# Optimization experiments

Measured on AMD Instinct MI355X. Metric: run time of the kernel, lower is better.

## Reference

```python
import jax, jax.numpy as jnp
import numpy as np

B, M, K, F_IN, H = 64, 1024, 16, 4, 64  # B graphs of M nodes each, k=16 neighbors


def _knn_idx(h):
    # h: [B, M, H] -> indices of K nearest neighbors (excluding self): [B, M, K]
    sq = jnp.sum(h * h, axis=-1)                                   # [B, M]
    d = sq[:, :, None] + sq[:, None, :] - 2.0 * jnp.einsum('bmf,bnf->bmn', h, h)
    d = jnp.where(jnp.eye(M, dtype=bool)[None], jnp.float32(jnp.inf), d)
    _, idx = jax.lax.top_k(-d, K)                                  # smallest distances
    return idx


def _edge_conv(h, w1, b1, w2, b2):
    # Dynamic-graph EdgeConv with max aggregation (PyG default):
    # msg = MLP(concat[x_i, x_j - x_i]); out_i = max_j msg
    idx = _knn_idx(h)                                              # [B, M, K]
    x_j = jax.vmap(lambda hb, ib: hb[ib])(h, idx)                  # [B, M, K, H]
    x_i = jnp.broadcast_to(h[:, :, None, :], x_j.shape)
    msg = jnp.concatenate([x_i, x_j - x_i], axis=-1)               # [B, M, K, 2H]
    msg = jax.nn.relu(msg @ w1 + b1) @ w2 + b2                     # [B, M, K, H]
    return jnp.max(msg, axis=2)                                    # [B, M, H]


def setup_inputs() -> dict:
    key = jax.random.key(0)
    ks = jax.random.split(key, 20)

    def lin(k, fi, fo):
        return jax.random.normal(k, (fi, fo), jnp.float32) / np.sqrt(fi)

    inp = {
        'x': jax.random.normal(ks[0], (B * M, F_IN), jnp.float32),
        'batch': jnp.repeat(jnp.arange(B, dtype=jnp.int64), M),
        # encoder: Linear(4,32) ReLU Linear(32,64) ReLU
        'enc_w1': lin(ks[1], F_IN, 32), 'enc_b1': jnp.zeros((32,), jnp.float32),
        'enc_w2': lin(ks[2], 32, H),    'enc_b2': jnp.zeros((H,), jnp.float32),
        # EdgeConv MLPs: Linear(128,64) ReLU Linear(64,64)
        'ec1_w1': lin(ks[3], 2 * H, H), 'ec1_b1': jnp.zeros((H,), jnp.float32),
        'ec1_w2': lin(ks[4], H, H),     'ec1_b2': jnp.zeros((H,), jnp.float32),
        'ec2_w1': lin(ks[5], 2 * H, H), 'ec2_b1': jnp.zeros((H,), jnp.float32),
        'ec2_w2': lin(ks[6], H, H),     'ec2_b2': jnp.zeros((H,), jnp.float32),
        # output MLP: Linear(64,32) ReLU Linear(32,1)
        'out_w1': lin(ks[7], H, 32),    'out_b1': jnp.zeros((32,), jnp.float32),
        'out_w2': lin(ks[8], 32, 1),    'out_b2': jnp.zeros((1,), jnp.float32),
    }
    return inp


def reference(x, batch, enc_w1, enc_b1, enc_w2, enc_b2,
              ec1_w1, ec1_b1, ec1_w2, ec1_b2,
              ec2_w1, ec2_b1, ec2_w2, ec2_b2,
              out_w1, out_b1, out_w2, out_b2):
    # batch is repeat(arange(B), M): equal-size graphs -> reshape into [B, M, .]
    h = jax.nn.relu(jax.nn.relu(x @ enc_w1 + enc_b1) @ enc_w2 + enc_b2)  # [N, 64]
    h = h.reshape(B, M, H)
    h = _edge_conv(h, ec1_w1, ec1_b1, ec1_w2, ec1_b2)
    h = _edge_conv(h, ec2_w1, ec2_b1, ec2_w2, ec2_b2)
    g = jnp.mean(h, axis=1)                                        # global_mean_pool -> [B, 64]
    out = jax.nn.relu(g @ out_w1 + out_b1) @ out_w2 + out_b2       # [B, 1]
    return out.reshape(-1)                                         # [B]
```

## Files before the change

kernel.cpp:

```cpp
#include <hip/hip_runtime.h>
#include <math.h>

#define B_ 64
#define M_ 1024
#define H_ 64
#define N_ (B_*M_)

typedef _Float16 half8 __attribute__((ext_vector_type(8)));
typedef float  floatx4 __attribute__((ext_vector_type(4)));

#define MFMA16(a,b,c) __builtin_amdgcn_mfma_f32_16x16x32_f16(a,b,c,0,0,0)
#define MED3(a,b,c)   __builtin_amdgcn_fmed3f(a,b,c)

__global__ __launch_bounds__(256) void enc_kernel(
    const float* __restrict__ x,
    const float* __restrict__ w1,
    const float* __restrict__ b1,
    const float* __restrict__ w2,
    const float* __restrict__ b2,
    float* __restrict__ h,
    _Float16* __restrict__ hhi,
    _Float16* __restrict__ hlo,
    float* __restrict__ sq)
{
    __shared__ float sw1[4*32];
    __shared__ float sb1[32];
    __shared__ float sw2[32*64];
    __shared__ float sb2[64];
    int t = threadIdx.x;
    for (int i = t; i < 128; i += 256) sw1[i] = w1[i];
    if (t < 32) sb1[t] = b1[t];
    for (int i = t; i < 2048; i += 256) sw2[i] = w2[i];
    if (t < 64) sb2[t] = b2[t];
    __syncthreads();
    int n = blockIdx.x * 256 + t;
    float4 xv = *(const float4*)(x + (size_t)n*4);
    float hid[32];
    #pragma unroll
    for (int o = 0; o < 32; ++o) {
        float a = sb1[o] + xv.x*sw1[0*32+o] + xv.y*sw1[1*32+o]
                        + xv.z*sw1[2*32+o] + xv.w*sw1[3*32+o];
        hid[o] = fmaxf(a, 0.f);
    }
    float* hout = h + (size_t)n*64;
    float sqa = 0.f;
    #pragma unroll 4
    for (int oc = 0; oc < 16; ++oc) {
        float4 acc = make_float4(sb2[oc*4+0], sb2[oc*4+1], sb2[oc*4+2], sb2[oc*4+3]);
        #pragma unroll
        for (int f = 0; f < 32; ++f) {
            float4 w = *(const float4*)(sw2 + f*64 + oc*4);
            float hv = hid[f];
            acc.x += hv*w.x; acc.y += hv*w.y; acc.z += hv*w.z; acc.w += hv*w.w;
        }
        acc.x = fmaxf(acc.x,0.f); acc.y = fmaxf(acc.y,0.f);
        acc.z = fmaxf(acc.z,0.f); acc.w = fmaxf(acc.w,0.f);
        *(float4*)(hout + oc*4) = acc;
        sqa += acc.x*acc.x + acc.y*acc.y + acc.z*acc.z + acc.w*acc.w;
        union { _Float16 f[4]; uint2 u; } Hh, Hl;
        Hh.f[0]=(_Float16)acc.x; Hh.f[1]=(_Float16)acc.y;
        Hh.f[2]=(_Float16)acc.z; Hh.f[3]=(_Float16)acc.w;
        Hl.f[0]=(_Float16)(acc.x-(float)Hh.f[0]); Hl.f[1]=(_Float16)(acc.y-(float)Hh.f[1]);
        Hl.f[2]=(_Float16)(acc.z-(float)Hh.f[2]); Hl.f[3]=(_Float16)(acc.w-(float)Hh.f[3]);
        *(uint2*)(hhi + (size_t)n*64 + oc*4) = Hh.u;
        *(uint2*)(hlo + (size_t)n*64 + oc*4) = Hl.u;
    }
    sq[n] = sqa;
}

__global__ __launch_bounds__(256) void convert_kernel(
    const float* __restrict__ h,
    _Float16* __restrict__ hhi, _Float16* __restrict__ hlo,
    float* __restrict__ sq)
{
    int t = threadIdx.x, lane = t & 63, w = t >> 6;
    int base = blockIdx.x * 64 + w * 16;
    for (int it = 0; it < 16; ++it) {
        int i = base + it;
        float v = h[(size_t)i*64 + lane];
        _Float16 hi = (_Float16)v;
        _Float16 lo = (_Float16)(v - (float)hi);
        hhi[(size_t)i*64 + lane] = hi;
        hlo[(size_t)i*64 + lane] = lo;
        float s = v*v;
        #pragma unroll
        for (int off = 1; off < 64; off <<= 1) s += __shfl_xor(s, off, 64);
        if (lane == 0) sq[i] = s;
    }
}

__global__ __launch_bounds__(256) void gemmA_kernel(
    const float* __restrict__ h,
    const float* __restrict__ w1,
    float* __restrict__ A)
{
    __shared__ float sw[64*64];
    int t = threadIdx.x;
    for (int idx = t; idx < 4096; idx += 256) sw[idx] = w1[4096 + idx];
    __syncthreads();
    int n = blockIdx.x * 256 + t;
    float4 hv[16];
    const float* src = h + (size_t)n*64;
    #pragma unroll
    for (int c = 0; c < 16; ++c) hv[c] = *(const float4*)(src + c*4);
    float* dst = A + (size_t)n*64;
    #pragma unroll 2
    for (int oc = 0; oc < 16; ++oc) {
        float4 acc = make_float4(0.f,0.f,0.f,0.f);
        #pragma unroll
        for (int f = 0; f < 64; ++f) {
            float xv = ((const float*)hv)[f];
            float4 w = *(const float4*)(sw + f*64 + oc*4);
            acc.x += xv*w.x; acc.y += xv*w.y; acc.z += xv*w.z; acc.w += xv*w.w;
        }
        *(float4*)(dst + oc*4) = acc;
    }
}

__global__ __launch_bounds__(512, 4) void knn_kernel(
    const _Float16* __restrict__ hhi,
    const _Float16* __restrict__ hlo,
    const float* __restrict__ sqg,
    unsigned short* __restrict__ knn)
{
    __shared__ __align__(16) _Float16 bufH[2][32*64];
    __shared__ __align__(16) _Float16 bufL[2][32*64];
    __shared__ __align__(16) float sqS[1024];
    __shared__ float md[128*65];

    int t = threadIdx.x, lane = t & 63, w = t >> 6;
    int bi = blockIdx.x;
    int g   = (bi & 7) | ((bi >> 6) << 3);
    int qt8 = (bi >> 3) & 7;
    const _Float16* hhig = hhi + (size_t)g*M_*64;
    const _Float16* hlog = hlo + (size_t)g*M_*64;
    const float*    sqb  = sqg + (size_t)g*M_;

    if (t < 256) ((float4*)sqS)[t] = ((const float4*)sqb)[t];

    int m16 = lane & 15, gid = lane >> 4;
    int crow = gid*4, koct = gid*8;
    int sw = m16 & 7;

    int u  = t & 255;
    int rr = u >> 3;
    int gl = u & 7;
    int pp = gl ^ (rr & 7);
    const _Float16* srcb = (t < 256 ? hhig : hlog) + rr*64 + gl*8;
    _Float16* dst0 = (t < 256 ? bufH[0] : bufL[0]) + rr*64 + pp*8;
    _Float16* dst1 = (t < 256 ? bufH[1] : bufL[1]) + rr*64 + pp*8;

    int qbase = qt8*128 + w*16;
    half8 Qh0, Qh1, Ql0, Ql1;
    {
        const _Float16* ph = hhig + (size_t)(qbase + m16)*64;
        const _Float16* pl = hlog + (size_t)(qbase + m16)*64;
        Qh0 = *(const half8*)(ph + koct);
        Qh1 = *(const half8*)(ph + 32 + koct);
        Ql0 = *(const half8*)(pl + koct);
        Ql1 = *(const half8*)(pl + 32 + koct);
    }

    float bd[16];
    #pragma unroll
    for (int k = 0; k < 16; ++k) bd[k] = INFINITY;

    int ts_self = qt8*8 + w;

    float4 a, b;
    a = *(const float4*)(srcb);
    b = *(const float4*)(srcb + 2048);
    *(float4*)dst0 = a;
    a = *(const float4*)(srcb + 2*2048);
    __syncthreads();

    float c1 = 1.f + sqS[qbase + m16];

    int o0 = m16*64 + ((gid ^ sw) * 8);
    int o1 = o0 ^ 32;

    auto insert4 = [&](floatx4 acc, float4 sqv, unsigned cid, bool st) {
        #pragma unroll
        for (int r = 0; r < 4; ++r) {
            float s  = fmaf(-2.f, acc[r], (&sqv.x)[r]);
            float t2 = c1 + s;
            unsigned kb = (__float_as_uint(t2) & 0xFFFFFC00u) | (cid + r);
            float fk = __uint_as_float(kb);
            if (st && (crow + r) == m16) fk = INFINITY;
            float nb0 = fminf(bd[0], fk);
            #pragma unroll
            for (int k = 15; k >= 1; --k) bd[k] = MED3(fk, bd[k-1], bd[k]);
            bd[0] = nb0;
        }
    };

    auto compute = [&](int T, const _Float16* bh, const _Float16* bl) {
        #pragma unroll
        for (int s = 0; s < 2; ++s) {
            int ob = s*1024;
            half8 Ah0 = *(const half8*)(bh + ob + o0);
            half8 Ah1 = *(const half8*)(bh + ob + o1);
            half8 Al0 = *(const half8*)(bl + ob + o0);
            half8 Al1 = *(const half8*)(bl + ob + o1);
            float4 sqv = *(const float4*)(sqS + T*32 + s*16 + crow);
            unsigned cid = (unsigned)(T*32 + s*16 + crow);
            bool st = (T*2 + s) == ts_self;
            floatx4 acc = {0.f, 0.f, 0.f, 0.f};
            acc = MFMA16(Ah0, Qh0, acc);
            acc = MFMA16(Ah1, Qh1, acc);
            acc = MFMA16(Ah0, Ql0, acc);
            acc = MFMA16(Ah1, Ql1, acc);
            acc = MFMA16(Al0, Qh0, acc);
            acc = MFMA16(Al1, Qh1, acc);
            insert4(acc, sqv, cid, st);
        }
    };

    #pragma unroll 1
    for (int T = 0; T < 32; T += 2) {
        __builtin_amdgcn_s_barrier();
        *(float4*)dst1 = b;
        b = *(const float4*)(srcb + (size_t)((T+3)&31)*2048);
        asm volatile("s_waitcnt lgkmcnt(0)" ::: "memory");
        __builtin_amdgcn_s_barrier();
        __builtin_amdgcn_sched_barrier(0);
        compute(T, bufH[0], bufL[0]);
        __builtin_amdgcn_s_barrier();
        *(float4*)dst0 = a;
        a = *(const float4*)(srcb + (size_t)((T+4)&31)*2048);
        asm volatile("s_waitcnt lgkmcnt(0)" ::: "memory");
        __builtin_amdgcn_s_barrier();
        __builtin_amdgcn_sched_barrier(0);
        compute(T+1, bufH[1], bufL[1]);
    }

    __syncthreads();
    int qrow = w*16 + m16;
    #pragma unroll
    for (int k = 0; k < 16; ++k) md[qrow*65 + gid*16 + k] = bd[k];
    __syncthreads();
    if (w < 2) {
        int q = w*64 + lane;
        float b2[16];
        #pragma unroll
        for (int k = 0; k < 16; ++k) b2[k] = INFINITY;
        const float* mrow = md + (size_t)q*65;
        #pragma unroll
        for (int c8 = 0; c8 < 8; ++c8) {
            float sv[8];
            #pragma unroll
            for (int j = 0; j < 8; ++j) sv[j] = mrow[c8*8 + j];
            #pragma unroll
            for (int j = 0; j < 8; ++j) {
                float s = sv[j];
                float nb0 = fminf(b2[0], s);
                #pragma unroll
                for (int k = 15; k >= 1; --k) b2[k] = MED3(s, b2[k-1], b2[k]);
                b2[0] = nb0;
            }
        }
        union { unsigned short us[16]; uint4 v4[2]; } o;
        #pragma unroll
        for (int k = 0; k < 16; ++k)
            o.us[k] = (unsigned short)(__float_as_uint(b2[k]) & 1023u);
        size_t gq = (size_t)g*M_ + qt8*128 + q;
        uint4* dst = (uint4*)(knn + gq*16);
        dst[0] = o.v4[0];
        dst[1] = o.v4[1];
    }
}

__global__ __launch_bounds__(256) void edge_kernel(
    const float* __restrict__ h,
    const float* __restrict__ A,
    const unsigned short* __restrict__ knn,
    const float* __restrict__ w1,
    const float* __restrict__ b1,
    const float* __restrict__ w2,
    const float* __restrict__ b2,
    float* __restrict__ hout)
{
    __shared__ __align__(16) _Float16 wdf[16*64*8];
    __shared__ __align__(16) _Float16 w2f[16*64*8];
    float* CsB = (float*)w2f;
    int t = threadIdx.x;
    for (int u = t; u < 512; u += 256) {
        int ulane = u & 63, nt = u >> 7, ks = (u >> 6) & 1;
        int n = nt*16 + (ulane & 15);
        int kbase = ks*32 + ((ulane >> 4) * 8);
        int fh = (((nt*2+ks)*2+0)*64 + ulane)*8;
        int fl = (((nt*2+ks)*2+1)*64 + ulane)*8;
        #pragma unroll
        for (int j = 0; j < 8; ++j) {
            int k = kbase + j;
            float vd = w1[k*64+n] - w1[4096 + k*64+n];
            _Float16 dh = (_Float16)vd;
            wdf[fh+j] = dh;
            wdf[fl+j] = (_Float16)(vd - (float)dh);
            float v2 = w2[k*64+n];
            _Float16 h2 = (_Float16)v2;
            w2f[fh+j] = h2;
            w2f[fl+j] = (_Float16)(v2 - (float)h2);
        }
    }
    __syncthreads();
    int lane = t & 63, wid = t >> 6;
    int m16 = lane & 15, gid = lane >> 4;
    int koct = gid*8, crow = gid*4;
    int bi = blockIdx.x;
    int g  = (bi & 7) | ((bi >> 7) << 3);
    int qt = (bi >> 3) & 15;
    int i0 = g*M_ + qt*64 + wid*16;
    const float* Ab = A + (size_t)g*M_*H_;

    half8 W2r[4][2][2];
    #pragma unroll
    for (int nt = 0; nt < 4; ++nt)
        #pragma unroll
        for (int ks = 0; ks < 2; ++ks)
            #pragma unroll
            for (int p = 0; p < 2; ++p)
                W2r[nt][ks][p] = *(const half8*)&w2f[(((nt*2+ks)*2+p)*64+lane)*8];

    float b1v[4];
    #pragma unroll
    for (int nt = 0; nt < 4; ++nt) b1v[nt] = b1[nt*16+m16];
    float b2v = b2[gid*16+m16];
    __syncthreads();

    half8 Hh[2], Hl[2];
    #pragma unroll
    for (int ks = 0; ks < 2; ++ks) {
        const float* hp = h + (size_t)(i0+m16)*64 + ks*32 + koct;
        float4 v0 = *(const float4*)hp;
        float4 v1 = *(const float4*)(hp+4);
        float va[8] = {v0.x,v0.y,v0.z,v0.w,v1.x,v1.y,v1.z,v1.w};
        #pragma unroll
        for (int j = 0; j < 8; ++j) {
            _Float16 hi = (_Float16)va[j];
            Hh[ks][j] = hi;
            Hl[ks][j] = (_Float16)(va[j]-(float)hi);
        }
    }
    #pragma unroll
    for (int nt = 0; nt < 4; ++nt) {
        floatx4 acc = {b1v[nt], b1v[nt], b1v[nt], b1v[nt]};
        #pragma unroll
        for (int ks = 0; ks < 2; ++ks) {
            half8 wh = *(const half8*)&wdf[(((nt*2+ks)*2+0)*64+lane)*8];
            half8 wl = *(const half8*)&wdf[(((nt*2+ks)*2+1)*64+lane)*8];
            acc = MFMA16(Hh[ks], wh, acc);
            acc = MFMA16(Hh[ks], wl, acc);
            acc = MFMA16(Hl[ks], wh, acc);
        }
        #pragma unroll
        for (int r = 0; r < 4; ++r)
            CsB[((wid*16) + crow + r)*64 + nt*16 + m16] = acc[r];
    }
    __syncthreads();

    const unsigned short* knb = knn + (size_t)i0*16;
    #pragma unroll 2
    for (int nn = 0; nn < 16; ++nn) {
        int j = knb[nn*16 + m16];
        const float* Ap = Ab + (size_t)j*64;
        half8 Mh[2], Ml[2];
        #pragma unroll
        for (int ks = 0; ks < 2; ++ks) {
            float4 a0 = *(const float4*)(Ap + ks*32 + koct);
            float4 a1 = *(const float4*)(Ap + ks*32 + koct + 4);
            const float* cp = &CsB[(wid*16 + nn)*64 + ks*32 + koct];
            float4 c0 = *(const float4*)cp;
            float4 c1 = *(const float4*)(cp+4);
            float mv[8] = {
                fmaxf(a0.x+c0.x,0.f), fmaxf(a0.y+c0.y,0.f),
                fmaxf(a0.z+c0.z,0.f), fmaxf(a0.w+c0.w,0.f),
                fmaxf(a1.x+c1.x,0.f), fmaxf(a1.y+c1.y,0.f),
                fmaxf(a1.z+c1.z,0.f), fmaxf(a1.w+c1.w,0.f)};
            #pragma unroll
            for (int jj = 0; jj < 8; ++jj) {
                _Float16 hi = (_Float16)mv[jj];
                Mh[ks][jj] = hi;
                Ml[ks][jj] = (_Float16)(mv[jj]-(float)hi);
            }
        }
        floatx4 acc[4];
        #pragma unroll
        for (int nt = 0; nt < 4; ++nt) {
            acc[nt] = (floatx4){0.f,0.f,0.f,0.f};
            #pragma unroll
            for (int ks = 0; ks < 2; ++ks) {
                acc[nt] = MFMA16(Mh[ks], W2r[nt][ks][0], acc[nt]);
                acc[nt] = MFMA16(Mh[ks], W2r[nt][ks][1], acc[nt]);
                acc[nt] = MFMA16(Ml[ks], W2r[nt][ks][0], acc[nt]);
            }
        }
        float om[4];
        #pragma unroll
        for (int nt = 0; nt < 4; ++nt) {
            float mr = fmaxf(fmaxf(acc[nt][0], acc[nt][1]),
                             fmaxf(acc[nt][2], acc[nt][3]));
            mr = fmaxf(mr, __shfl_xor(mr, 16, 64));
            mr = fmaxf(mr, __shfl_xor(mr, 32, 64));
            om[nt] = mr;
        }
        float val = (gid == 0) ? om[0] : (gid == 1) ? om[1]
                  : (gid == 2) ? om[2] : om[3];
        hout[(size_t)(i0+nn)*64 + gid*16 + m16] = val + b2v;
    }
}

__global__ __launch_bounds__(256) void pool_kernel(
    const float* __restrict__ h,
    const float* __restrict__ w1,
    const float* __restrict__ b1,
    const float* __restrict__ w2,
    const float* __restrict__ b2,
    float* __restrict__ out)
{
    __shared__ float part[4][64];
    __shared__ float g[64];
    __shared__ float hid[32];
    int t = threadIdx.x;
    int o = t & 63, p = t >> 6;
    int b = blockIdx.x;
    const float* hb = h + (size_t)b*M_*H_;
    float s = 0.f;
    for (int m = p; m < M_; m += 4) s += hb[(size_t)m*64 + o];
    part[p][o] = s;
    __syncthreads();
    if (t < 64) g[t] = (part[0][t] + part[1][t] + part[2][t] + part[3][t]) * (1.f/M_);
    __syncthreads();
    if (t < 32) {
        float a = b1[t];
        for (int f = 0; f < 64; ++f) a += g[f] * w1[f*32 + t];
        hid[t] = fmaxf(a, 0.f);
    }
    __syncthreads();
    if (t == 0) {
        float a = b2[0];
        for (int f = 0; f < 32; ++f) a += hid[f] * w2[f];
        out[b] = a;
    }
}

extern "C" void kernel_launch(void* const* d_in, const int* in_sizes, int n_in,
                              void* d_out, int out_size, void* d_ws, size_t ws_size,
                              hipStream_t stream)
{
    (void)in_sizes; (void)n_in; (void)out_size; (void)ws_size;
    const float* x      = (const float*)d_in[0];
    const float* enc_w1 = (const float*)d_in[2];
    const float* enc_b1 = (const float*)d_in[3];
    const float* enc_w2 = (const float*)d_in[4];
    const float* enc_b2 = (const float*)d_in[5];
    const float* ec1_w1 = (const float*)d_in[6];
    const float* ec1_b1 = (const float*)d_in[7];
    const float* ec1_w2 = (const float*)d_in[8];
    const float* ec1_b2 = (const float*)d_in[9];
    const float* ec2_w1 = (const float*)d_in[10];
    const float* ec2_b1 = (const float*)d_in[11];
    const float* ec2_w2 = (const float*)d_in[12];
    const float* ec2_b2 = (const float*)d_in[13];
    const float* out_w1 = (const float*)d_in[14];
    const float* out_b1 = (const float*)d_in[15];
    const float* out_w2 = (const float*)d_in[16];
    const float* out_b2 = (const float*)d_in[17];

    char* ws = (char*)d_ws;
    float*          h   = (float*)(ws);
    char*           r2  = ws + (size_t)N_*64*4;
    _Float16*       hhi = (_Float16*)r2;
    _Float16*       hlo = (_Float16*)(r2 + (size_t)N_*64*2);
    float*          A   = (float*)r2;
    unsigned short* idx = (unsigned short*)(ws + (size_t)N_*64*4*2);
    float*          sq  = (float*)(ws + (size_t)N_*64*4*2 + (size_t)N_*16*2);

    enc_kernel<<<N_/256, 256, 0, stream>>>(x, enc_w1, enc_b1, enc_w2, enc_b2,
                                           h, hhi, hlo, sq);
    knn_kernel <<<B_*8, 512, 0, stream>>>(hhi, hlo, sq, idx);
    gemmA_kernel<<<N_/256, 256, 0, stream>>>(h, ec1_w1, A);
    edge_kernel<<<N_/64, 256, 0, stream>>>(h, A, idx, ec1_w1, ec1_b1, ec1_w2, ec1_b2, h);
    convert_kernel<<<N_/64, 256, 0, stream>>>(h, hhi, hlo, sq);
    knn_kernel <<<B_*8, 512, 0, stream>>>(hhi, hlo, sq, idx);
    gemmA_kernel<<<N_/256, 256, 0, stream>>>(h, ec2_w1, A);
    edge_kernel<<<N_/64, 256, 0, stream>>>(h, A, idx, ec2_w1, ec2_b1, ec2_w2, ec2_b2, h);
    pool_kernel<<<B_, 256, 0, stream>>>(h, out_w1, out_b1, out_w2, out_b2, (float*)d_out);
}
```

Before: 404.1 us.

## Double candidate tile to 64 rows and use one barrier per kNN stage

The kNN kernel now stages 64 candidate rows per LDS buffer instead of 32, so the loop runs 16 iterations with 4 MFMA sub-tiles each. Each iteration writes the next tile into the other buffer while computing on the current one, and ends with a single barrier instead of two per tile. This halves the number of barriers and loop iterations and overlaps the LDS stores with compute. In exchange it doubles LDS usage for the staging buffers, which may lower occupancy, and keeps more global-load registers live.

New measurement: 403.2 us. About the same (-0.2%).

```diff
diff --git a/kernel.cpp b/kernel.cpp
--- a/kernel.cpp
+++ b/kernel.cpp
@@ -123,8 +123,8 @@
     const float* __restrict__ sqg,
     unsigned short* __restrict__ knn)
 {
-    __shared__ __align__(16) _Float16 bufH[2][32*64];
-    __shared__ __align__(16) _Float16 bufL[2][32*64];
+    __shared__ __align__(16) _Float16 bufH[2][64*64];
+    __shared__ __align__(16) _Float16 bufL[2][64*64];
     __shared__ __align__(16) float sqS[1024];
     __shared__ float md[128*65];
 
@@ -147,8 +147,8 @@
     int gl = u & 7;
     int pp = gl ^ (rr & 7);
     const _Float16* srcb = (t < 256 ? hhig : hlog) + rr*64 + gl*8;
-    _Float16* dst0 = (t < 256 ? bufH[0] : bufL[0]) + rr*64 + pp*8;
-    _Float16* dst1 = (t < 256 ? bufH[1] : bufL[1]) + rr*64 + pp*8;
+    _Float16* dstA = (t < 256 ? bufH[0] : bufL[0]) + rr*64 + pp*8;
+    _Float16* dstB = (t < 256 ? bufH[1] : bufL[1]) + rr*64 + pp*8;
 
     int qbase = qt8*128 + w*16;
     half8 Qh0, Qh1, Ql0, Ql1;
@@ -167,11 +167,11 @@
 
     int ts_self = qt8*8 + w;
 
-    float4 a, b;
-    a = *(const float4*)(srcb);
-    b = *(const float4*)(srcb + 2048);
-    *(float4*)dst0 = a;
-    a = *(const float4*)(srcb + 2*2048);
+    float4 p0 = *(const float4*)(srcb);
+    float4 p1 = *(const float4*)(srcb + 2048);
+    *(float4*)dstA = p0;  *(float4*)(dstA + 2048) = p1;
+    p0 = *(const float4*)(srcb + 4096);
+    p1 = *(const float4*)(srcb + 4096 + 2048);
     __syncthreads();
 
     float c1 = 1.f + sqS[qbase + m16];
@@ -196,15 +196,15 @@
 
     auto compute = [&](int T, const _Float16* bh, const _Float16* bl) {
         #pragma unroll
-        for (int s = 0; s < 2; ++s) {
+        for (int s = 0; s < 4; ++s) {
             int ob = s*1024;
             half8 Ah0 = *(const half8*)(bh + ob + o0);
             half8 Ah1 = *(const half8*)(bh + ob + o1);
             half8 Al0 = *(const half8*)(bl + ob + o0);
             half8 Al1 = *(const half8*)(bl + ob + o1);
-            float4 sqv = *(const float4*)(sqS + T*32 + s*16 + crow);
-            unsigned cid = (unsigned)(T*32 + s*16 + crow);
-            bool st = (T*2 + s) == ts_self;
+            float4 sqv = *(const float4*)(sqS + T*64 + s*16 + crow);
+            unsigned cid = (unsigned)(T*64 + s*16 + crow);
+            bool st = (T*4 + s) == ts_self;
             floatx4 acc = {0.f, 0.f, 0.f, 0.f};
             acc = MFMA16(Ah0, Qh0, acc);
             acc = MFMA16(Ah1, Qh1, acc);
@@ -217,24 +217,20 @@
     };
 
     #pragma unroll 1
-    for (int T = 0; T < 32; T += 2) {
-        __builtin_amdgcn_s_barrier();
-        *(float4*)dst1 = b;
-        b = *(const float4*)(srcb + (size_t)((T+3)&31)*2048);
+    for (int T = 0; T < 16; ++T) {
+        __builtin_amdgcn_sched_barrier(0);
+        _Float16* dw = (T & 1) ? dstA : dstB;
+        *(float4*)dw = p0;  *(float4*)(dw + 2048) = p1;
+        { size_t o = (size_t)((T+2)&15)*4096;
+          p0 = *(const float4*)(srcb + o);
+          p1 = *(const float4*)(srcb + o + 2048); }
+        const _Float16* bh = (T & 1) ? bufH[1] : bufH[0];
+        const _Float16* bl = (T & 1) ? bufL[1] : bufL[0];
+        compute(T, bh, bl);
         asm volatile("s_waitcnt lgkmcnt(0)" ::: "memory");
         __builtin_amdgcn_s_barrier();
-        __builtin_amdgcn_sched_barrier(0);
-        compute(T, bufH[0], bufL[0]);
-        __builtin_amdgcn_s_barrier();
-        *(float4*)dst0 = a;
-        a = *(const float4*)(srcb + (size_t)((T+4)&31)*2048);
-        asm volatile("s_waitcnt lgkmcnt(0)" ::: "memory");
-        __builtin_amdgcn_s_barrier();
-        __builtin_amdgcn_sched_barrier(0);
-        compute(T+1, bufH[1], bufL[1]);
-    }
-
-    __syncthreads();
+    }
+
     int qrow = w*16 + m16;
     #pragma unroll
     for (int k = 0; k < 16; ++k) md[qrow*65 + gid*16 + k] = bd[k];
```

## Shrink kNN blocks to 256 threads and merge top-k lists with shuffles

Applied to the files above, without the earlier changes.

The kNN kernel now uses 256-thread blocks covering 64 queries each, twice as many blocks, with each thread loading both the hi and lo fp16 tiles. The candidate-tile pipeline becomes one barrier per tile: the next tile is prefetched into registers while the current one is computed. The shared-memory merge of the four per-lane top-16 lists is replaced by two rounds of xor-shuffle exchange plus a bitonic merge in registers. The aim is to cut shared memory and barrier cost and raise occupancy, in exchange for reloading each graph's candidate data in twice as many blocks.

After: 411.0 us. Within noise of the previous version (+1.7%).

```diff
diff --git a/kernel.cpp b/kernel.cpp
--- a/kernel.cpp
+++ b/kernel.cpp
@@ -117,7 +117,7 @@
     }
 }
 
-__global__ __launch_bounds__(512, 4) void knn_kernel(
+__global__ __launch_bounds__(256, 6) void knn_kernel(
     const _Float16* __restrict__ hhi,
     const _Float16* __restrict__ hlo,
     const float* __restrict__ sqg,
@@ -126,31 +126,30 @@
     __shared__ __align__(16) _Float16 bufH[2][32*64];
     __shared__ __align__(16) _Float16 bufL[2][32*64];
     __shared__ __align__(16) float sqS[1024];
-    __shared__ float md[128*65];
 
     int t = threadIdx.x, lane = t & 63, w = t >> 6;
     int bi = blockIdx.x;
-    int g   = (bi & 7) | ((bi >> 6) << 3);
-    int qt8 = (bi >> 3) & 7;
+    int g  = (bi & 7) | ((bi >> 7) << 3);
+    int qt = (bi >> 3) & 15;
     const _Float16* hhig = hhi + (size_t)g*M_*64;
     const _Float16* hlog = hlo + (size_t)g*M_*64;
     const float*    sqb  = sqg + (size_t)g*M_;
 
-    if (t < 256) ((float4*)sqS)[t] = ((const float4*)sqb)[t];
+    ((float4*)sqS)[t] = ((const float4*)sqb)[t];
 
     int m16 = lane & 15, gid = lane >> 4;
     int crow = gid*4, koct = gid*8;
     int sw = m16 & 7;
 
-    int u  = t & 255;
-    int rr = u >> 3;
-    int gl = u & 7;
+    int rr = t >> 3;
+    int gl = t & 7;
     int pp = gl ^ (rr & 7);
-    const _Float16* srcb = (t < 256 ? hhig : hlog) + rr*64 + gl*8;
-    _Float16* dst0 = (t < 256 ? bufH[0] : bufL[0]) + rr*64 + pp*8;
-    _Float16* dst1 = (t < 256 ? bufH[1] : bufL[1]) + rr*64 + pp*8;
-
-    int qbase = qt8*128 + w*16;
+    const _Float16* srcH = hhig + rr*64 + gl*8;
+    const _Float16* srcL = hlog + rr*64 + gl*8;
+    _Float16* dstH = bufH[0] + rr*64 + pp*8;
+    _Float16* dstL = bufL[0] + rr*64 + pp*8;
+
+    int qbase = qt*64 + w*16;
     half8 Qh0, Qh1, Ql0, Ql1;
     {
         const _Float16* ph = hhig + (size_t)(qbase + m16)*64;
@@ -165,13 +164,14 @@
     #pragma unroll
     for (int k = 0; k < 16; ++k) bd[k] = INFINITY;
 
-    int ts_self = qt8*8 + w;
-
-    float4 a, b;
-    a = *(const float4*)(srcb);
-    b = *(const float4*)(srcb + 2048);
-    *(float4*)dst0 = a;
-    a = *(const float4*)(srcb + 2*2048);
+    int ts_self = qt*4 + w;
+
+    {
+        float4 h0 = *(const float4*)srcH;
+        float4 l0 = *(const float4*)srcL;
+        *(float4*)dstH = h0;
+        *(float4*)dstL = l0;
+    }
     __syncthreads();
 
     float c1 = 1.f + sqS[qbase + m16];
@@ -217,53 +217,47 @@
     };
 
     #pragma unroll 1
-    for (int T = 0; T < 32; T += 2) {
-        __builtin_amdgcn_s_barrier();
-        *(float4*)dst1 = b;
-        b = *(const float4*)(srcb + (size_t)((T+3)&31)*2048);
+    for (int T = 0; T < 32; ++T) {
+        size_t o = (size_t)((T+1) & 31) * 2048;
+        float4 h1 = *(const float4*)(srcH + o);
+        float4 l1 = *(const float4*)(srcL + o);
+        const _Float16* bh = (T & 1) ? bufH[1] : bufH[0];
+        const _Float16* bl = (T & 1) ? bufL[1] : bufL[0];
+        compute(T, bh, bl);
+        int sel = ((T & 1) ^ 1) * 2048;
+        *(float4*)(dstH + sel) = h1;
+        *(float4*)(dstL + sel) = l1;
         asm volatile("s_waitcnt lgkmcnt(0)" ::: "memory");
         __builtin_amdgcn_s_barrier();
-        __builtin_amdgcn_sched_barrier(0);
-        compute(T, bufH[0], bufL[0]);
-        __builtin_amdgcn_s_barrier();
-        *(float4*)dst0 = a;
-        a = *(const float4*)(srcb + (size_t)((T+4)&31)*2048);
-        asm volatile("s_waitcnt lgkmcnt(0)" ::: "memory");
-        __builtin_amdgcn_s_barrier();
-        __builtin_amdgcn_sched_barrier(0);
-        compute(T+1, bufH[1], bufL[1]);
-    }
-
-    __syncthreads();
-    int qrow = w*16 + m16;
-    #pragma unroll
-    for (int k = 0; k < 16; ++k) md[qrow*65 + gid*16 + k] = bd[k];
-    __syncthreads();
-    if (w < 2) {
-        int q = w*64 + lane;
-        float b2[16];
-        #pragma unroll
-        for (int k = 0; k < 16; ++k) b2[k] = INFINITY;
-        const float* mrow = md + (size_t)q*65;
-        #pragma unroll
-        for (int c8 = 0; c8 < 8; ++c8) {
-            float sv[8];
+    }
+
+    #pragma unroll
+    for (int rnd = 0; rnd < 2; ++rnd) {
+        float rv[16], m[16];
+        #pragma unroll
+        for (int k = 0; k < 16; ++k) rv[k] = __shfl_xor(bd[k], 16 << rnd, 64);
+        #pragma unroll
+        for (int k = 0; k < 16; ++k) m[k] = fminf(bd[k], rv[15-k]);
+        #pragma unroll
+        for (int s = 8; s >= 1; s >>= 1) {
             #pragma unroll
-            for (int j = 0; j < 8; ++j) sv[j] = mrow[c8*8 + j];
-            #pragma unroll
-            for (int j = 0; j < 8; ++j) {
-                float s = sv[j];
-                float nb0 = fminf(b2[0], s);
-                #pragma unroll
-                for (int k = 15; k >= 1; --k) b2[k] = MED3(s, b2[k-1], b2[k]);
-                b2[0] = nb0;
+            for (int i = 0; i < 16; ++i) {
+                if ((i & s) == 0) {
+                    float lo = fminf(m[i], m[i+s]);
+                    float hi = fmaxf(m[i], m[i+s]);
+                    m[i] = lo; m[i+s] = hi;
+                }
             }
         }
+        #pragma unroll
+        for (int k = 0; k < 16; ++k) bd[k] = m[k];
+    }
+    if (gid == 0) {
         union { unsigned short us[16]; uint4 v4[2]; } o;
         #pragma unroll
         for (int k = 0; k < 16; ++k)
-            o.us[k] = (unsigned short)(__float_as_uint(b2[k]) & 1023u);
-        size_t gq = (size_t)g*M_ + qt8*128 + q;
+            o.us[k] = (unsigned short)(__float_as_uint(bd[k]) & 1023u);
+        size_t gq = (size_t)g*M_ + qt*64 + w*16 + m16;
         uint4* dst = (uint4*)(knn + gq*16);
         dst[0] = o.v4[0];
         dst[1] = o.v4[1];
@@ -478,11 +472,11 @@
 
     enc_kernel<<<N_/256, 256, 0, stream>>>(x, enc_w1, enc_b1, enc_w2, enc_b2,
                                            h, hhi, hlo, sq);
-    knn_kernel <<<B_*8, 512, 0, stream>>>(hhi, hlo, sq, idx);
+    knn_kernel <<<B_*16, 256, 0, stream>>>(hhi, hlo, sq, idx);
     gemmA_kernel<<<N_/256, 256, 0, stream>>>(h, ec1_w1, A);
     edge_kernel<<<N_/64, 256, 0, stream>>>(h, A, idx, ec1_w1, ec1_b1, ec1_w2, ec1_b2, h);
     convert_kernel<<<N_/64, 256, 0, stream>>>(h, hhi, hlo, sq);
-    knn_kernel <<<B_*8, 512, 0, stream>>>(hhi, hlo, sq, idx);
+    knn_kernel <<<B_*16, 256, 0, stream>>>(hhi, hlo, sq, idx);
     gemmA_kernel<<<N_/256, 256, 0, stream>>>(h, ec2_w1, A);
     edge_kernel<<<N_/64, 256, 0, stream>>>(h, A, idx, ec2_w1, ec2_b1, ec2_w2, ec2_b2, h);
     pool_kernel<<<B_, 256, 0, stream>>>(h, out_w1, out_b1, out_w2, out_b2, (float*)d_out);
```
